# Kernel tuning notes

Hardware: AMD Instinct MI355X
Metric: run time of the kernel (lower is better)

## Reference

```python
import jax, jax.numpy as jnp
import numpy as np
import math

B, C, H, W = 8, 256, 64, 64
G = 32           # norm_groups
IMG_C = 3        # image_channels * wavelet_components
EPS = 1e-5


def group_norm(x, gamma, beta):
    # x: [B, C, H, W]; normalize over (C//G, H, W) within each of G groups
    b, c, h, w = x.shape
    xg = x.reshape(b, G, c // G, h, w)
    mean = xg.mean(axis=(2, 3, 4), keepdims=True)
    var = xg.var(axis=(2, 3, 4), keepdims=True)
    xg = (xg - mean) * jax.lax.rsqrt(var + EPS)
    x = xg.reshape(b, c, h, w)
    return x * gamma[None, :, None, None] + beta[None, :, None, None]


def conv1x1(x, weight):
    # weight: [out_c, in_c]; 1x1 conv == channel matmul
    return jnp.einsum('oc,bchw->bohw', weight, x)


def setup_inputs() -> dict:
    key = jax.random.key(0)
    ks = jax.random.split(key, 8)
    s_q = 1.0 / math.sqrt(IMG_C)
    s_kv = 1.0 / math.sqrt(C)
    return {
        'input': jax.random.normal(ks[0], (B, C, H, W), jnp.float32),
        'quary': jax.random.normal(ks[1], (B, IMG_C, H, W), jnp.float32),
        'gn_weight': jnp.ones((C,), jnp.float32),
        'gn_bias': jnp.zeros((C,), jnp.float32),
        'w_q': jax.random.uniform(ks[2], (C, IMG_C), jnp.float32, -s_q, s_q),
        'w_kv': jax.random.uniform(ks[3], (2 * C, C), jnp.float32, -s_kv, s_kv),
        'w_out': jax.random.uniform(ks[4], (C, C), jnp.float32, -s_kv, s_kv),
        'b_out': jax.random.uniform(ks[5], (C,), jnp.float32, -s_kv, s_kv),
    }


def reference(input, quary, gn_weight, gn_bias, w_q, w_kv, w_out, b_out):
    b, c, h, w = input.shape
    norm = group_norm(input, gn_weight, gn_bias)
    kv = conv1x1(norm, w_kv)                      # [B, 2C, H, W]
    key_t, value = kv[:, :c], kv[:, c:]           # each [B, C, H, W]
    q = conv1x1(quary, w_q)                       # [B, C, H, W]
    # attention over all spatial positions, single head, head_dim = C
    attn = jnp.einsum('bchw,bcyx->bhwyx', q, key_t) / math.sqrt(c)
    attn = jax.nn.softmax(attn.reshape(b, h, w, h * w), axis=-1)
    attn = attn.reshape(b, h, w, h, w)
    out = jnp.einsum('bhwyx,bcyx->bchw', attn, value)  # [B, C, H, W]
    out = conv1x1(out, w_out) + b_out[None, :, None, None]
    return out + input
```

## Files before the change

### kernel.cpp

```cpp
#include <hip/hip_runtime.h>

typedef unsigned short u16;
typedef unsigned int   u32;
typedef float  f32x4  __attribute__((ext_vector_type(4)));
typedef float  fltx4  __attribute__((ext_vector_type(4)));
typedef float  f32x2  __attribute__((ext_vector_type(2)));
typedef short  bf16x8 __attribute__((ext_vector_type(8)));
typedef u32    u32x4  __attribute__((ext_vector_type(4)));
typedef u32    u32x2  __attribute__((ext_vector_type(2)));

#define CDIM 256
#define NPIX 4096
#define QSCALE 0.09016843736f

__device__ __forceinline__ u16 f2bf(float f) {
  u32 u = __builtin_bit_cast(u32, f);
  u += 0x7fffu + ((u >> 16) & 1u);
  return (u16)(u >> 16);
}
__device__ __forceinline__ float bf2f(u16 h) {
  return __builtin_bit_cast(float, (u32)h << 16);
}

#if __has_builtin(__builtin_amdgcn_exp2f)
#define FEXP2 __builtin_amdgcn_exp2f
#else
#define FEXP2 exp2f
#endif

#define LO2(v) __builtin_shufflevector(v, v, 0, 1)
#define HI2(v) __builtin_shufflevector(v, v, 2, 3)

union U8 { bf16x8 v; u16 u[8]; u32 w[4]; };

__device__ __forceinline__ void llds16(u16* lds_base, const u16* gsrc) {
  __builtin_amdgcn_global_load_lds(
      (const __attribute__((address_space(1))) unsigned int*)gsrc,
      (__attribute__((address_space(3))) unsigned int*)lds_base, 16, 0, 0);
}

__global__ __launch_bounds__(1024) void gn_stats_prep(
    const float* __restrict__ x, const float* __restrict__ wkv,
    const float* __restrict__ wout, const float* __restrict__ wq,
    float* __restrict__ stats, u16* __restrict__ w16, float* __restrict__ wq3p) {
  const int bid = blockIdx.x, tid = threadIdx.x;
  if (bid < 256) {
    const float* base = x + (long)bid * 32768;
    float s = 0.f, s2 = 0.f;
    for (int i = tid; i < 8192; i += 1024) {
      fltx4 v = ((const fltx4*)base)[i];
      s  += v[0] + v[1] + v[2] + v[3];
      s2 += v[0]*v[0] + v[1]*v[1] + v[2]*v[2] + v[3]*v[3];
    }
    for (int off = 1; off < 64; off <<= 1) {
      s  += __shfl_xor(s, off);
      s2 += __shfl_xor(s2, off);
    }
    __shared__ float red[32];
    int w = tid >> 6;
    if ((tid & 63) == 0) { red[w] = s; red[16 + w] = s2; }
    __syncthreads();
    if (tid < 16) {
      s  = red[tid];
      s2 = red[16 + tid];
      for (int off = 1; off < 16; off <<= 1) {
        s  += __shfl_xor(s, off);
        s2 += __shfl_xor(s2, off);
      }
      if (tid == 0) {
        float mean = s * (1.f / 32768.f);
        float var  = s2 * (1.f / 32768.f) - mean * mean;
        stats[bid * 2]     = mean;
        stats[bid * 2 + 1] = rsqrtf(var + 1e-5f);
      }
    }
    return;
  }
  const int blk = bid - 256;
  if (blk < 4) {
    const float* s = (blk < 2 ? wkv + 65536 : wout) + (blk & 1) * 32768;
    u16* d = w16 + (blk >> 1) * 65536 + (blk & 1) * 32768;
    for (int i = tid * 4; i < 32768; i += 4096) {
      fltx4 v = *(const fltx4*)(s + i);
      u32x2 o;
      o[0] = (u32)f2bf(v[0]) | ((u32)f2bf(v[1]) << 16);
      o[1] = (u32)f2bf(v[2]) | ((u32)f2bf(v[3]) << 16);
      *(u32x2*)(d + i) = o;
    }
  } else if (tid < 256) {
    const int p = blk - 4, c = tid;
    float a0 = 0.f, a1 = 0.f, a2 = 0.f;
    for (int o = p * 64; o < p * 64 + 64; ++o) {
      float kv = wkv[o * 256 + c];
      a0 += wq[o * 3 + 0] * kv;
      a1 += wq[o * 3 + 1] * kv;
      a2 += wq[o * 3 + 2] * kv;
    }
    float* dst = wq3p + (p * 256 + c) * 4;
    dst[0] = a0 * QSCALE; dst[1] = a1 * QSCALE; dst[2] = a2 * QSCALE; dst[3] = 0.f;
  }
}

#define TSTR 264
__global__ __launch_bounds__(256) void gn_fused(const float* __restrict__ x,
                                                const float* __restrict__ stats,
                                                const float* __restrict__ gamma,
                                                const float* __restrict__ beta,
                                                const float* __restrict__ wq3p,
                                                const u16* __restrict__ w16v,
                                                u16* __restrict__ Vv,
                                                float* __restrict__ K3x,
                                                float* __restrict__ K3y,
                                                float* __restrict__ K3z) {
  __shared__ u16 tile[64 * TSTR];
  __shared__ float wl4[256 * 4];
  __shared__ float part[4][64][4];
  const int tid = threadIdx.x;
  const int b = blockIdx.y, nb = blockIdx.x * 64;
  const int nIn = tid & 63, c4 = tid >> 6;
  const int lane = tid & 63;
  const int m = lane & 15, quad = lane >> 4;
  {
    const f32x4* wp = (const f32x4*)wq3p;
    *(f32x4*)&wl4[tid * 4] = wp[tid] + wp[256 + tid] + wp[512 + tid] + wp[768 + tid];
  }
  const float* xb = x + (long)b * (CDIM * NPIX);
  #pragma unroll
  for (int p8 = 0; p8 < 8; ++p8) {
    U8 pk;
    #pragma unroll
    for (int e = 0; e < 8; ++e) {
      int c = c4 * 64 + p8 * 8 + e;
      int g = c >> 3;
      float mean = stats[(b * 32 + g) * 2];
      float rstd = stats[(b * 32 + g) * 2 + 1];
      float v = xb[(long)c * NPIX + nb + nIn];
      pk.u[e] = f2bf((v - mean) * rstd * gamma[c] + beta[c]);
    }
    *(bf16x8*)&tile[nIn * TSTR + c4 * 64 + p8 * 8] = pk.v;
  }
  __syncthreads();
  {
    float a0 = 0.f, a1 = 0.f, a2 = 0.f;
    #pragma unroll
    for (int p8 = 0; p8 < 8; ++p8) {
      U8 v; v.v = *(const bf16x8*)&tile[nIn * TSTR + c4 * 64 + p8 * 8];
      #pragma unroll
      for (int e = 0; e < 8; ++e) {
        int c = c4 * 64 + p8 * 8 + e;
        float f = bf2f(v.u[e]);
        const f32x4 wv = *(const f32x4*)&wl4[c * 4];
        a0 += f * wv[0]; a1 += f * wv[1]; a2 += f * wv[2];
      }
    }
    part[c4][nIn][0] = a0; part[c4][nIn][1] = a1; part[c4][nIn][2] = a2;
  }
  __syncthreads();
  if (c4 == 0) {
    float s0 = part[0][nIn][0] + part[1][nIn][0] + part[2][nIn][0] + part[3][nIn][0];
    float s1 = part[0][nIn][1] + part[1][nIn][1] + part[2][nIn][1] + part[3][nIn][1];
    float s2 = part[0][nIn][2] + part[1][nIn][2] + part[2][nIn][2] + part[3][nIn][2];
    long idx = (long)b * NPIX + nb + nIn;
    K3x[idx] = s0; K3y[idx] = s1; K3z[idx] = s2;
  }
  f32x4 acc[4][4] = {};
  #pragma unroll
  for (int ks = 0; ks < 8; ++ks) {
    const int kb = ks * 32;
    bf16x8 av[4], bv[4];
    #pragma unroll
    for (int i = 0; i < 4; ++i)
      av[i] = *(const bf16x8*)&w16v[(c4 * 64 + i * 16 + m) * 256 + kb + quad * 8];
    #pragma unroll
    for (int i = 0; i < 4; ++i)
      bv[i] = *(const bf16x8*)&tile[(i * 16 + m) * TSTR + kb + quad * 8];
    #pragma unroll
    for (int mi = 0; mi < 4; ++mi)
      #pragma unroll
      for (int ni = 0; ni < 4; ++ni)
        acc[mi][ni] = __builtin_amdgcn_mfma_f32_16x16x32_bf16(av[mi], bv[ni], acc[mi][ni], 0, 0, 0);
  }
  u16* Vb = Vv + (long)b * (CDIM * NPIX);
  #pragma unroll
  for (int mi = 0; mi < 4; ++mi)
    #pragma unroll
    for (int r = 0; r < 4; ++r) {
      int o = c4 * 64 + mi * 16 + quad * 4 + r;
      #pragma unroll
      for (int ni = 0; ni < 4; ++ni)
        Vb[(long)o * NPIX + nb + ni * 16 + m] = f2bf(acc[mi][ni][r]);
    }
}

__global__ __launch_bounds__(256, 4) void gemm_out(
    const u16* __restrict__ Ap, const u16* __restrict__ B0,
    const u16* __restrict__ B1, const float* __restrict__ ls,
    float* __restrict__ out, const float* __restrict__ bias,
    const float* __restrict__ resid) {
  __shared__ u16 Als[64 * 64];
  __shared__ u16 Bls[128 * 64];
  __shared__ float invB[128];
  const int tid = threadIdx.x;
  const int lane = tid & 63;
  const int w = tid >> 6;
  const int m = lane & 15, quad = lane >> 4;
  const int wm = w & 1, wn = w >> 1;
  const int m0 = blockIdx.x * 64, n0 = blockIdx.y * 128;
  const int bz = blockIdx.z;
  const long S = (long)NPIX * CDIM;

  if (tid < 128) {
    long n = (long)bz * 4096 + n0 + tid;
    invB[tid] = 1.f / (ls[n] + ls[32768 + n]);
  }
  __syncthreads();

  const int slotOff = ((lane & 7) ^ (lane >> 3)) * 8;
  int srcA[2], srcB[4];
  #pragma unroll
  for (int it = 0; it < 2; ++it) {
    int row = (w * 2 + it) * 8 + (lane >> 3);
    srcA[it] = (m0 + row) * CDIM + slotOff;
  }
  #pragma unroll
  for (int it = 0; it < 4; ++it) {
    int row = (w * 4 + it) * 8 + (lane >> 3);
    srcB[it] = (n0 + row) * CDIM + slotOff;
  }

  f32x4 acc[2][4] = {};

  #pragma unroll
  for (int ks = 0; ks < 8; ++ks) {
    const int kb = (ks & 3) * 64;
    const u16* Bsrc = (ks < 4 ? B0 : B1) + S * bz;
    if (ks) __syncthreads();
    #pragma unroll
    for (int it = 0; it < 2; ++it)
      llds16(Als + (w * 2 + it) * 512, Ap + srcA[it] + kb);
    #pragma unroll
    for (int it = 0; it < 4; ++it)
      llds16(Bls + (w * 4 + it) * 512, Bsrc + (long)srcB[it] + kb);
    __syncthreads();
    #pragma unroll
    for (int s = 0; s < 2; ++s) {
      const int chunk = ((s * 4 + quad) ^ (m & 7)) * 8;
      bf16x8 av[2], bv[4];
      #pragma unroll
      for (int i = 0; i < 2; ++i)
        av[i] = *(const bf16x8*)&Als[(wm * 32 + i * 16 + m) * 64 + chunk];
      #pragma unroll
      for (int i = 0; i < 4; ++i)
        bv[i] = *(const bf16x8*)&Bls[(wn * 64 + i * 16 + m) * 64 + chunk];
      #pragma unroll
      for (int mi = 0; mi < 2; ++mi)
        #pragma unroll
        for (int ni = 0; ni < 4; ++ni)
          acc[mi][ni] = __builtin_amdgcn_mfma_f32_16x16x32_bf16(av[mi], bv[ni], acc[mi][ni], 0, 0, 0);
    }
  }

  const int row0 = m0 + wm * 32;
  const int col0 = n0 + wn * 64 + m;
  float* ob = out + S * bz;
  const float* res = resid + S * bz;
  float iv[4];
  #pragma unroll
  for (int ni = 0; ni < 4; ++ni)
    iv[ni] = invB[wn * 64 + ni * 16 + m];
  #pragma unroll
  for (int mi = 0; mi < 2; ++mi)
    #pragma unroll
    for (int r = 0; r < 4; ++r) {
      int row = row0 + mi * 16 + quad * 4 + r;
      float bs = bias[row];
      #pragma unroll
      for (int ni = 0; ni < 4; ++ni) {
        long off = (long)row * NPIX + col0 + ni * 16;
        ob[off] = acc[mi][ni][r] * iv[ni] + bs + res[off];
      }
    }
}

#define MFMA16(a, bfr, c) __builtin_amdgcn_mfma_f32_16x16x32_bf16(a, bfr, c, 0, 0, 0)

#define P_LOAD(ks, JB)                                                      \
  {                                                                         \
    const int jo_ = (JB) + (ks) * 32 + quad * 8;                            \
    kx0 = *(const fltx4*)(Kx + jo_); kx1 = *(const fltx4*)(Kx + jo_ + 4);   \
    ky0 = *(const fltx4*)(Ky + jo_); ky1 = *(const fltx4*)(Ky + jo_ + 4);   \
    kz0 = *(const fltx4*)(Kz + jo_); kz1 = *(const fltx4*)(Kz + jo_ + 4);   \
  }

#define P_EXP(PB, ks)                                                       \
  {                                                                         \
    f32x2 xc_[4] = {LO2(kx0), HI2(kx0), LO2(kx1), HI2(kx1)};                \
    f32x2 yc_[4] = {LO2(ky0), HI2(ky0), LO2(ky1), HI2(ky1)};                \
    f32x2 zc_[4] = {LO2(kz0), HI2(kz0), LO2(kz1), HI2(kz1)};                \
    _Pragma("unroll")                                                       \
    for (int qm_ = 0; qm_ < 2; ++qm_) {                                     \
      _Pragma("unroll")                                                     \
      for (int c2_ = 0; c2_ < 4; ++c2_) {                                   \
        f32x2 s_ = xc_[c2_] * y2[qm_][0] + yc_[c2_] * y2[qm_][1]            \
                 + zc_[c2_] * y2[qm_][2];                                   \
        float p0_ = FEXP2(s_[0]);                                           \
        float p1_ = FEXP2(s_[1]);                                           \
        u32 r0_ = __builtin_bit_cast(u32, p0_) + 0x8000u;                   \
        u32 r1_ = __builtin_bit_cast(u32, p1_) + 0x8000u;                   \
        PB[qm_][ks].w[c2_] = (r0_ >> 16) | (r1_ & 0xffff0000u);             \
        f32x2 pv_; pv_[0] = p0_; pv_[1] = p1_;                              \
        lsv[qm_] += pv_;                                                    \
      }                                                                     \
    }                                                                       \
  }

#define PV_GROUP(PB, CT0)                                                   \
  _Pragma("unroll")                                                         \
  for (int ct_ = (CT0); ct_ < (CT0) + 4; ++ct_) {                           \
    int c_ = ct_ * 16 + m;                                                  \
    bf16x8 a0_ = *(const bf16x8*)&Vb[c_ * 64 + (((quad)     ^ (c_ & 7)) << 3)]; \
    bf16x8 a1_ = *(const bf16x8*)&Vb[c_ * 64 + (((4 + quad) ^ (c_ & 7)) << 3)]; \
    acc[0][ct_] = MFMA16(a0_, PB[0][0].v, acc[0][ct_]);                     \
    acc[1][ct_] = MFMA16(a0_, PB[1][0].v, acc[1][ct_]);                     \
    acc[0][ct_] = MFMA16(a1_, PB[0][1].v, acc[0][ct_]);                     \
    acc[1][ct_] = MFMA16(a1_, PB[1][1].v, acc[1][ct_]);                     \
  }

__global__ __launch_bounds__(256, 2) void attn_kernel(
    const float* __restrict__ quary,
    const float* __restrict__ K3x, const float* __restrict__ K3y,
    const float* __restrict__ K3z,
    const u16* __restrict__ V, u16* __restrict__ Op0, u16* __restrict__ Op1,
    float* __restrict__ lsum) {
  __shared__ u16 VLS[2][256 * 64];
  const int lane = threadIdx.x & 63, w = threadIdx.x >> 6;
  const int m = lane & 15, quad = lane >> 4;
  const int b = blockIdx.z, half = blockIdx.y;
  const int qb = blockIdx.x * 128 + w * 32;

  f32x2 y2[2][3];
  #pragma unroll
  for (int qm = 0; qm < 2; ++qm) {
    int n = qb + qm * 16 + m;
    float q0 = quary[b * 12288 + n];
    float q1 = quary[b * 12288 + 4096 + n];
    float q2 = quary[b * 12288 + 8192 + n];
    y2[qm][0][0] = q0; y2[qm][0][1] = q0;
    y2[qm][1][0] = q1; y2[qm][1][1] = q1;
    y2[qm][2][0] = q2; y2[qm][2][1] = q2;
  }

  const float* Kx = K3x + (long)b * NPIX + half * 2048;
  const float* Ky = K3y + (long)b * NPIX + half * 2048;
  const float* Kz = K3z + (long)b * NPIX + half * 2048;
  const u16* VG = V + (long)b * CDIM * NPIX + half * 2048;

  int srcV[8];
  #pragma unroll
  for (int i = 0; i < 8; ++i) {
    int c = (w * 8 + i) * 8 + (lane >> 3);
    srcV[i] = c * NPIX + (((lane & 7) ^ (c & 7)) << 3);
  }

  f32x2 lsv[2] = {};
  f32x4 acc[2][16] = {};
  U8 pbA[2][2], pbB[2][2];
  fltx4 kx0, kx1, ky0, ky1, kz0, kz1;

  #pragma unroll
  for (int i = 0; i < 8; ++i)
    llds16(VLS[0] + (w * 8 + i) * 512, VG + srcV[i]);

  P_LOAD(0, 0); P_EXP(pbA, 0);
  P_LOAD(1, 0); P_EXP(pbA, 1);

  for (int kt = 0; kt < 31; ++kt) {
    __syncthreads();
    #pragma unroll
    for (int i = 0; i < 8; ++i)
      llds16(VLS[(kt + 1) & 1] + (w * 8 + i) * 512, VG + srcV[i] + (kt + 1) * 64);
    const u16* Vb = VLS[kt & 1];
    const int JB = (kt + 1) * 64;

    P_LOAD(0, JB);
    PV_GROUP(pbA, 0);
    PV_GROUP(pbA, 4);
    P_EXP(pbB, 0);
    P_LOAD(1, JB);
    PV_GROUP(pbA, 8);
    PV_GROUP(pbA, 12);
    P_EXP(pbB, 1);

    pbA[0][0] = pbB[0][0]; pbA[0][1] = pbB[0][1];
    pbA[1][0] = pbB[1][0]; pbA[1][1] = pbB[1][1];
  }
  {
    __syncthreads();
    const u16* Vb = VLS[1];
    PV_GROUP(pbA, 0);
    PV_GROUP(pbA, 4);
    PV_GROUP(pbA, 8);
    PV_GROUP(pbA, 12);
  }

  u16* OpB = (half ? Op1 : Op0);
  #pragma unroll
  for (int qm = 0; qm < 2; ++qm) {
    int n = qb + qm * 16 + m;
    u16* row = OpB + ((long)b * NPIX + n) * CDIM + quad * 4;
    #pragma unroll
    for (int ct = 0; ct < 16; ++ct) {
      u32x2 o;
      o[0] = (u32)f2bf(acc[qm][ct][0]) | ((u32)f2bf(acc[qm][ct][1]) << 16);
      o[1] = (u32)f2bf(acc[qm][ct][2]) | ((u32)f2bf(acc[qm][ct][3]) << 16);
      *(u32x2*)(row + ct * 16) = o;
    }
    float ls = lsv[qm][0] + lsv[qm][1];
    ls += __shfl_xor(ls, 16);
    ls += __shfl_xor(ls, 32);
    if (lane < 16)
      lsum[(long)half * 32768 + (long)b * NPIX + n] = ls;
  }
}

extern "C" void kernel_launch(void* const* d_in, const int* in_sizes, int n_in,
                              void* d_out, int out_size, void* d_ws, size_t ws_size,
                              hipStream_t stream) {
  (void)in_sizes; (void)n_in; (void)out_size; (void)ws_size;
  const float* input = (const float*)d_in[0];
  const float* quary = (const float*)d_in[1];
  const float* gnw   = (const float*)d_in[2];
  const float* gnb   = (const float*)d_in[3];
  const float* wq    = (const float*)d_in[4];
  const float* wkv   = (const float*)d_in[5];
  const float* wout  = (const float*)d_in[6];
  const float* bout  = (const float*)d_in[7];
  float* out = (float*)d_out;

  char* ws = (char*)d_ws;
  float* stats = (float*)ws;
  float* wq3p  = (float*)(ws + 4096);
  float* lsum  = (float*)(ws + 20480);
  float* K3x   = (float*)(ws + 282624);
  float* K3y   = (float*)(ws + 413696);
  float* K3z   = (float*)(ws + 544768);
  u16* w16   = (u16*)(ws + 675840);
  const long base = 937984;
  u16* Vv    = (u16*)(ws + base);
  u16* Op0   = (u16*)(ws + base + 1L * 16777216);
  u16* Op1   = (u16*)(ws + base + 2L * 16777216);

  gn_stats_prep<<<264, 1024, 0, stream>>>(input, wkv, wout, wq, stats, w16, wq3p);
  gn_fused<<<dim3(64, 8), 256, 0, stream>>>(input, stats, gnw, gnb, wq3p,
                                            w16, Vv, K3x, K3y, K3z);
  attn_kernel<<<dim3(32, 2, 8), 256, 0, stream>>>(quary, K3x, K3y, K3z, Vv, Op0, Op1, lsum);
  gemm_out<<<dim3(4, 32, 8), 256, 0, stream>>>(
      w16 + 65536, Op0, Op1, lsum, out, bout, input);
}
```

Measured before the change: 231.2 us.

## Double-buffer gemm_out LDS tiles and stage V-projection stores through LDS

The output GEMM now keeps two LDS buffers for A and B, so the next K-slice loads while the current one feeds MFMA, and one barrier per iteration replaces two. Separately, the V projection kernel writes its bf16 results into the shared tile first and then stores them to global memory as 16-byte coalesced rows instead of scattered 2-byte writes. The trade-off is double the LDS in gemm_out, which may limit occupancy under launch_bounds(256,4), plus extra barriers in the projection kernel. The correctness of invB visibility now depends on the first loop-iteration barrier.

After: 233.6 us. No clear change (+1.0%).

```diff
diff --git a/kernel.cpp b/kernel.cpp
--- a/kernel.cpp
+++ b/kernel.cpp
@@ -180,7 +180,7 @@
       for (int ni = 0; ni < 4; ++ni)
         acc[mi][ni] = __builtin_amdgcn_mfma_f32_16x16x32_bf16(av[mi], bv[ni], acc[mi][ni], 0, 0, 0);
   }
-  u16* Vb = Vv + (long)b * (CDIM * NPIX);
+  __syncthreads();
   #pragma unroll
   for (int mi = 0; mi < 4; ++mi)
     #pragma unroll
@@ -188,8 +188,17 @@
       int o = c4 * 64 + mi * 16 + quad * 4 + r;
       #pragma unroll
       for (int ni = 0; ni < 4; ++ni)
-        Vb[(long)o * NPIX + nb + ni * 16 + m] = f2bf(acc[mi][ni][r]);
-    }
+        tile[o * 64 + ni * 16 + m] = f2bf(acc[mi][ni][r]);
+    }
+  __syncthreads();
+  u16* Vb = Vv + (long)b * (CDIM * NPIX);
+  #pragma unroll
+  for (int it = 0; it < 8; ++it) {
+    int idx = it * 256 + tid;
+    int o = idx >> 3;
+    int n8 = (idx & 7) * 8;
+    *(u32x4*)&Vb[(long)o * NPIX + nb + n8] = *(const u32x4*)&tile[o * 64 + n8];
+  }
 }
 
 __global__ __launch_bounds__(256, 4) void gemm_out(
@@ -197,8 +206,8 @@
     const u16* __restrict__ B1, const float* __restrict__ ls,
     float* __restrict__ out, const float* __restrict__ bias,
     const float* __restrict__ resid) {
-  __shared__ u16 Als[64 * 64];
-  __shared__ u16 Bls[128 * 64];
+  __shared__ u16 Als[2][64 * 64];
+  __shared__ u16 Bls[2][128 * 64];
   __shared__ float invB[128];
   const int tid = threadIdx.x;
   const int lane = tid & 63;
@@ -213,7 +222,6 @@
     long n = (long)bz * 4096 + n0 + tid;
     invB[tid] = 1.f / (ls[n] + ls[32768 + n]);
   }
-  __syncthreads();
 
   const int slotOff = ((lane & 7) ^ (lane >> 3)) * 8;
   int srcA[2], srcB[4];
@@ -230,28 +238,41 @@
 
   f32x4 acc[2][4] = {};
 
+  {
+    const u16* Bsrc = B0 + S * bz;
+    #pragma unroll
+    for (int it = 0; it < 2; ++it)
+      llds16(Als[0] + (w * 2 + it) * 512, Ap + srcA[it]);
+    #pragma unroll
+    for (int it = 0; it < 4; ++it)
+      llds16(Bls[0] + (w * 4 + it) * 512, Bsrc + (long)srcB[it]);
+  }
+
   #pragma unroll
   for (int ks = 0; ks < 8; ++ks) {
-    const int kb = (ks & 3) * 64;
-    const u16* Bsrc = (ks < 4 ? B0 : B1) + S * bz;
-    if (ks) __syncthreads();
-    #pragma unroll
-    for (int it = 0; it < 2; ++it)
-      llds16(Als + (w * 2 + it) * 512, Ap + srcA[it] + kb);
-    #pragma unroll
-    for (int it = 0; it < 4; ++it)
-      llds16(Bls + (w * 4 + it) * 512, Bsrc + (long)srcB[it] + kb);
     __syncthreads();
+    if (ks < 7) {
+      const int kb = ((ks + 1) & 3) * 64;
+      const u16* Bsrc = ((ks + 1) < 4 ? B0 : B1) + S * bz;
+      #pragma unroll
+      for (int it = 0; it < 2; ++it)
+        llds16(Als[(ks + 1) & 1] + (w * 2 + it) * 512, Ap + srcA[it] + kb);
+      #pragma unroll
+      for (int it = 0; it < 4; ++it)
+        llds16(Bls[(ks + 1) & 1] + (w * 4 + it) * 512, Bsrc + (long)srcB[it] + kb);
+    }
+    const u16* Ab = Als[ks & 1];
+    const u16* Bb = Bls[ks & 1];
     #pragma unroll
     for (int s = 0; s < 2; ++s) {
       const int chunk = ((s * 4 + quad) ^ (m & 7)) * 8;
       bf16x8 av[2], bv[4];
       #pragma unroll
       for (int i = 0; i < 2; ++i)
-        av[i] = *(const bf16x8*)&Als[(wm * 32 + i * 16 + m) * 64 + chunk];
+        av[i] = *(const bf16x8*)&Ab[(wm * 32 + i * 16 + m) * 64 + chunk];
       #pragma unroll
       for (int i = 0; i < 4; ++i)
-        bv[i] = *(const bf16x8*)&Bls[(wn * 64 + i * 16 + m) * 64 + chunk];
+        bv[i] = *(const bf16x8*)&Bb[(wn * 64 + i * 16 + m) * 64 + chunk];
       #pragma unroll
       for (int mi = 0; mi < 2; ++mi)
         #pragma unroll
```
